# Optimization experiments

Measured on AMD Instinct MI355X. Metric: run time of the kernel, lower is better.

The kernel has to match this reference:

```python
import jax, jax.numpy as jnp
import numpy as np

VOCAB = 100000
EMBED = 64
SENT = 20
MEM = 50
BATCH = 32
HOPS = 3
PAD_ID = 0


def position_encoding(sentence_size, embedding_size):
    # Section 4.1 of MemN2N paper, vectorized. Returns [sentence_size, embedding_size].
    i = np.arange(1, embedding_size + 1, dtype=np.float32)[:, None]   # [E,1]
    j = np.arange(1, sentence_size + 1, dtype=np.float32)[None, :]    # [1,S]
    enc = (i - (embedding_size + 1) / 2.0) * (j - (sentence_size + 1) / 2.0)
    enc = 1.0 + 4.0 * enc / embedding_size / sentence_size
    enc[:, -1] = 1.0
    return jnp.asarray(enc.T, dtype=jnp.float32)  # [S,E]


def setup_inputs() -> dict:
    key = jax.random.key(0)
    k1, k2, k3, k4 = jax.random.split(key, 4)
    stories = jax.random.randint(k1, (BATCH, MEM, SENT), 0, VOCAB, dtype=jnp.int64 if jax.config.jax_enable_x64 else jnp.int32)
    queries = jax.random.randint(k2, (BATCH, SENT), 0, VOCAB, dtype=jnp.int64 if jax.config.jax_enable_x64 else jnp.int32)
    A = jax.random.normal(k3, (VOCAB, EMBED), dtype=jnp.float32) * 0.1
    C = jax.random.normal(k4, (HOPS, VOCAB, EMBED), dtype=jnp.float32) * 0.1
    # padding_idx=PAD_ID rows are zero, as in nn.Embedding(padding_idx=...)
    A = A.at[PAD_ID].set(0.0)
    C = C.at[:, PAD_ID].set(0.0)
    encoding = position_encoding(SENT, EMBED)
    return {"stories": stories, "queries": queries, "A": A, "C": C, "encoding": encoding}


def reference(stories, queries, A, C, encoding):
    # queries: [B,S], stories: [B,M,S], A: [V,E], C: [hops,V,E], encoding: [S,E]
    q_emb = A[queries]                                # [B,S,E]
    u = (q_emb * encoding).sum(axis=1)                # [B,E]
    for hop in range(HOPS):
        table_in = A if hop == 0 else C[hop - 1]
        emb_A = table_in[stories]                     # [B,M,S,E]
        m = (emb_A * encoding).sum(axis=2)            # [B,M,E]
        dotted = jnp.einsum('bme,be->bm', m, u)       # [B,M]
        probs = jax.nn.softmax(dotted, axis=-1)       # [B,M]
        emb_C = C[hop][stories]                       # [B,M,S,E]
        c = (emb_C * encoding).sum(axis=2)            # [B,M,E]
        o = jnp.einsum('bm,bme->be', probs, c)        # [B,E]
        u = u + o
    return u @ C[-1].T                                # [B,V]
```

## Files before the change

kernel.cpp:

```cpp
#include <hip/hip_runtime.h>
#include <hip/hip_bf16.h>

#define VOCAB 100000
#define EMBED 64
#define SENT  20
#define MEM   50
#define BATCH 32
#define HOPS  3

#define NSET   4
#define NSLOTB (NSET * MEM)
#define LDSP   65

__device__ __forceinline__ float bfr(unsigned short x) {
    union { unsigned int u; float f; } cv;
    cv.u = ((unsigned int)x) << 16;
    return cv.f;
}

__device__ __forceinline__ bool is_bf16(const void* enc) {
    return ((const unsigned int*)enc)[639] == 0x3F803F80u;
}

template<bool BF>
__device__ __forceinline__ float ldT(const void* p, size_t idx) {
    if constexpr (BF) return bfr(((const unsigned short*)p)[idx]);
    else              return ((const float*)p)[idx];
}

__device__ __forceinline__ float wave_sum(float d) {
#pragma unroll
    for (int off = 32; off > 0; off >>= 1) d += __shfl_xor(d, off, 64);
    return d;
}

template<bool BF>
__device__ __forceinline__ void gather_all(const int* __restrict__ stories,
                                           const int* __restrict__ queries,
                                           const void* __restrict__ A,
                                           const void* __restrict__ C,
                                           const void* __restrict__ enc,
                                           float* __restrict__ mc,
                                           float* __restrict__ uls,
                                           int b)
{
    const int tid = threadIdx.x;
    const int e   = tid & 63;
    const int w   = tid >> 6;
    const size_t VE = (size_t)VOCAB * EMBED;

    float encr[SENT];
#pragma unroll
    for (int s = 0; s < SENT; ++s) encr[s] = ldT<BF>(enc, s * EMBED + e);

    for (int slot = w; slot < NSLOTB + 1; slot += 16) {
        if (slot < NSLOTB) {
            const int t  = slot / MEM;
            const int mm = slot % MEM;
            const void* T   = (t == 0) ? A : C;
            const size_t to = (t == 0) ? 0 : (size_t)(t - 1) * VE;

            int wst = (e < SENT) ? stories[(b * MEM + mm) * SENT + e] : 0;
            float acc = 0.f;
#pragma unroll
            for (int s = 0; s < SENT; ++s) {
                int wd = __shfl(wst, s, 64);
                acc += ldT<BF>(T, to + (size_t)wd * EMBED + e) * encr[s];
            }
            mc[(t * MEM + mm) * LDSP + e] = acc;
        } else {
            int wq = (e < SENT) ? queries[b * SENT + e] : 0;
            float u = 0.f;
#pragma unroll
            for (int s = 0; s < SENT; ++s) {
                int wd = __shfl(wq, s, 64);
                u += ldT<BF>(A, (size_t)wd * EMBED + e) * encr[s];
            }
            uls[e] = u;
        }
    }
}

__global__ __launch_bounds__(1024) void k_front(
    const int* __restrict__ stories,
    const int* __restrict__ queries,
    const void* __restrict__ A,
    const void* __restrict__ C,
    const void* __restrict__ enc,
    float* __restrict__ u3g)
{
    __shared__ float mc[NSET * MEM * LDSP];
    __shared__ float uls[EMBED];
    __shared__ float ols[4][EMBED];

    const bool bf = is_bf16(enc);
    const int b   = blockIdx.x;
    const int tid = threadIdx.x;

    if (bf) gather_all<true >(stories, queries, A, C, enc, mc, uls, b);
    else    gather_all<false>(stories, queries, A, C, enc, mc, uls, b);
    __syncthreads();

    const int lane = tid & 63;
    const int widx = tid >> 6;

    for (int hop = 0; hop < HOPS; ++hop) {
        if (tid < 256) {
            float d = 0.f;
            if (lane < MEM) {
                const float* row = mc + (hop * MEM + lane) * LDSP;
#pragma unroll
                for (int e2 = 0; e2 < EMBED; ++e2) d += row[e2] * uls[e2];
            }
            float x  = (lane < MEM) ? d : -3.4e38f;
            float mx = x;
#pragma unroll
            for (int off = 32; off > 0; off >>= 1) mx = fmaxf(mx, __shfl_xor(mx, off, 64));
            float ex = (lane < MEM) ? __expf(x - mx) : 0.f;
            float sm = wave_sum(ex);
            float p  = ex / sm;

            float o = 0.f;
            const float* crow = mc + ((hop + 1) * MEM) * LDSP;
#pragma unroll
            for (int k = 0; k < 13; ++k) {
                int mm = widx * 13 + k;
                if (mm < MEM)
                    o += __shfl(p, mm, 64) * crow[mm * LDSP + lane];
            }
            ols[widx][lane] = o;
        }
        __syncthreads();
        if (tid < EMBED)
            uls[tid] += ols[0][tid] + ols[1][tid] + ols[2][tid] + ols[3][tid];
        __syncthreads();
    }

    if (tid < EMBED) u3g[b * EMBED + tid] = uls[tid];
}

template<bool BF>
__device__ __forceinline__ void out_one(const float* __restrict__ su,
                                        const void* __restrict__ Cbase,
                                        void* __restrict__ out, int v)
{
    const size_t c2_off = (size_t)2 * VOCAB * EMBED;
    float row[EMBED];
    if constexpr (BF) {
        const uint4* rp = (const uint4*)((const unsigned short*)Cbase + c2_off + (size_t)v * EMBED);
#pragma unroll
        for (int i = 0; i < 8; ++i) {
            uint4 r = rp[i];
            row[i*8 + 0] = bfr((unsigned short)(r.x & 0xffff));
            row[i*8 + 1] = bfr((unsigned short)(r.x >> 16));
            row[i*8 + 2] = bfr((unsigned short)(r.y & 0xffff));
            row[i*8 + 3] = bfr((unsigned short)(r.y >> 16));
            row[i*8 + 4] = bfr((unsigned short)(r.z & 0xffff));
            row[i*8 + 5] = bfr((unsigned short)(r.z >> 16));
            row[i*8 + 6] = bfr((unsigned short)(r.w & 0xffff));
            row[i*8 + 7] = bfr((unsigned short)(r.w >> 16));
        }
    } else {
        const float4* rp = (const float4*)((const float*)Cbase + c2_off + (size_t)v * EMBED);
#pragma unroll
        for (int i = 0; i < 16; ++i) {
            float4 r = rp[i];
            row[i*4 + 0] = r.x; row[i*4 + 1] = r.y;
            row[i*4 + 2] = r.z; row[i*4 + 3] = r.w;
        }
    }

    float res[BATCH];
#pragma unroll
    for (int bb = 0; bb < BATCH; ++bb) {
        const float4* sp = (const float4*)(su + bb * EMBED);
        float acc = 0.f;
#pragma unroll
        for (int e4 = 0; e4 < 16; ++e4) {
            float4 us = sp[e4];
            acc += row[e4*4+0]*us.x + row[e4*4+1]*us.y
                 + row[e4*4+2]*us.z + row[e4*4+3]*us.w;
        }
        res[bb] = acc;
    }

    if constexpr (BF) {
        unsigned short* ob = (unsigned short*)out;
#pragma unroll
        for (int bb = 0; bb < BATCH; ++bb) {
            __hip_bfloat16 h = __float2bfloat16(res[bb]);
            ob[(size_t)bb * VOCAB + v] = *(unsigned short*)&h;
        }
    } else {
        float* of = (float*)out;
#pragma unroll
        for (int bb = 0; bb < BATCH; ++bb)
            of[(size_t)bb * VOCAB + v] = res[bb];
    }
}

__global__ __launch_bounds__(256) void k_out(const float* __restrict__ u,
                                             const void* __restrict__ Cbase,
                                             const void* __restrict__ enc,
                                             void* __restrict__ out)
{
    const bool bf = is_bf16(enc);
    __shared__ __align__(16) float su[BATCH * EMBED];
    for (int i = threadIdx.x; i < BATCH * EMBED; i += 256) su[i] = u[i];
    __syncthreads();
    const int v = blockIdx.x * 256 + threadIdx.x;
    if (v >= VOCAB) return;
    if (bf) out_one<true >(su, Cbase, enc ? out : out, v);
    else    out_one<false>(su, Cbase, out, v);
}

extern "C" void kernel_launch(void* const* d_in, const int* in_sizes, int n_in,
                              void* d_out, int out_size, void* d_ws, size_t ws_size,
                              hipStream_t stream)
{
    const int*  stories = (const int*)d_in[0];
    const int*  queries = (const int*)d_in[1];
    const void* A       = d_in[2];
    const void* C       = d_in[3];
    const void* enc     = d_in[4];

    float* u3g = (float*)d_ws;

    k_front<<<BATCH, 1024, 0, stream>>>(stories, queries, A, C, enc, u3g);
    k_out<<<(VOCAB + 255) / 256, 256, 0, stream>>>(u3g, C, enc, d_out);
}
```

Baseline: 169.7 us.

## Merge front and output kernels into one cooperative kernel with grid-wide gather

Replaces the two-kernel pipeline (32-block gather+hops kernel, then vocab projection) with a single cooperative kernel of 512 blocks. The embedding gather is spread across all 2048 waves instead of 32 blocks, with results written to a global workspace. Two grid.sync barriers separate the gather, the per-batch hop computation on 32 blocks, and the vocab projection. This removes one kernel launch and the under-parallelised gather, at the cost of grid-sync overhead, global-memory round trips for the memory vectors, and a 512-block grid covering only about 391 output tiles.

```diff
diff --git a/kernel.cpp b/kernel.cpp
--- a/kernel.cpp
+++ b/kernel.cpp
@@ -1,5 +1,8 @@
 #include <hip/hip_runtime.h>
 #include <hip/hip_bf16.h>
+#include <hip/hip_cooperative_groups.h>
+
+namespace cg = cooperative_groups;
 
 #define VOCAB 100000
 #define EMBED 64
@@ -9,8 +12,9 @@
 #define HOPS  3
 
 #define NSET   4
-#define NSLOTB (NSET * MEM)
-#define LDSP   65
+#define NSLOT  (NSET * BATCH * MEM)
+#define GRID   512
+#define NWAVES (GRID * 4)
 
 __device__ __forceinline__ float bfr(unsigned short x) {
     union { unsigned int u; float f; } cv;
@@ -35,108 +39,50 @@
 }
 
 template<bool BF>
-__device__ __forceinline__ void gather_all(const int* __restrict__ stories,
-                                           const int* __restrict__ queries,
-                                           const void* __restrict__ A,
-                                           const void* __restrict__ C,
-                                           const void* __restrict__ enc,
-                                           float* __restrict__ mc,
-                                           float* __restrict__ uls,
-                                           int b)
+__device__ __forceinline__ void phase1(const int* __restrict__ stories,
+                                       const int* __restrict__ queries,
+                                       const void* __restrict__ A,
+                                       const void* __restrict__ C,
+                                       const void* __restrict__ enc,
+                                       float* __restrict__ mc_ws,
+                                       float* __restrict__ u0g)
 {
     const int tid = threadIdx.x;
     const int e   = tid & 63;
-    const int w   = tid >> 6;
+    const int gw  = blockIdx.x * 4 + (tid >> 6);
     const size_t VE = (size_t)VOCAB * EMBED;
 
     float encr[SENT];
 #pragma unroll
     for (int s = 0; s < SENT; ++s) encr[s] = ldT<BF>(enc, s * EMBED + e);
 
-    for (int slot = w; slot < NSLOTB + 1; slot += 16) {
-        if (slot < NSLOTB) {
-            const int t  = slot / MEM;
-            const int mm = slot % MEM;
+    for (int slot = gw; slot < NSLOT + BATCH; slot += NWAVES) {
+        if (slot < NSLOT) {
+            const int t  = slot / (BATCH * MEM);
+            const int bm = slot % (BATCH * MEM);
             const void* T   = (t == 0) ? A : C;
             const size_t to = (t == 0) ? 0 : (size_t)(t - 1) * VE;
 
-            int wst = (e < SENT) ? stories[(b * MEM + mm) * SENT + e] : 0;
+            int wst = (e < SENT) ? stories[bm * SENT + e] : 0;
             float acc = 0.f;
 #pragma unroll
             for (int s = 0; s < SENT; ++s) {
-                int wd = __shfl(wst, s, 64);
-                acc += ldT<BF>(T, to + (size_t)wd * EMBED + e) * encr[s];
-            }
-            mc[(t * MEM + mm) * LDSP + e] = acc;
+                int w = __shfl(wst, s, 64);
+                acc += ldT<BF>(T, to + (size_t)w * EMBED + e) * encr[s];
+            }
+            mc_ws[slot * EMBED + e] = acc;
         } else {
+            const int b = slot - NSLOT;
             int wq = (e < SENT) ? queries[b * SENT + e] : 0;
             float u = 0.f;
 #pragma unroll
             for (int s = 0; s < SENT; ++s) {
-                int wd = __shfl(wq, s, 64);
-                u += ldT<BF>(A, (size_t)wd * EMBED + e) * encr[s];
-            }
-            uls[e] = u;
-        }
-    }
-}
-
-__global__ __launch_bounds__(1024) void k_front(
-    const int* __restrict__ stories,
-    const int* __restrict__ queries,
-    const void* __restrict__ A,
-    const void* __restrict__ C,
-    const void* __restrict__ enc,
-    float* __restrict__ u3g)
-{
-    __shared__ float mc[NSET * MEM * LDSP];
-    __shared__ float uls[EMBED];
-    __shared__ float ols[4][EMBED];
-
-    const bool bf = is_bf16(enc);
-    const int b   = blockIdx.x;
-    const int tid = threadIdx.x;
-
-    if (bf) gather_all<true >(stories, queries, A, C, enc, mc, uls, b);
-    else    gather_all<false>(stories, queries, A, C, enc, mc, uls, b);
-    __syncthreads();
-
-    const int lane = tid & 63;
-    const int widx = tid >> 6;
-
-    for (int hop = 0; hop < HOPS; ++hop) {
-        if (tid < 256) {
-            float d = 0.f;
-            if (lane < MEM) {
-                const float* row = mc + (hop * MEM + lane) * LDSP;
-#pragma unroll
-                for (int e2 = 0; e2 < EMBED; ++e2) d += row[e2] * uls[e2];
-            }
-            float x  = (lane < MEM) ? d : -3.4e38f;
-            float mx = x;
-#pragma unroll
-            for (int off = 32; off > 0; off >>= 1) mx = fmaxf(mx, __shfl_xor(mx, off, 64));
-            float ex = (lane < MEM) ? __expf(x - mx) : 0.f;
-            float sm = wave_sum(ex);
-            float p  = ex / sm;
-
-            float o = 0.f;
-            const float* crow = mc + ((hop + 1) * MEM) * LDSP;
-#pragma unroll
-            for (int k = 0; k < 13; ++k) {
-                int mm = widx * 13 + k;
-                if (mm < MEM)
-                    o += __shfl(p, mm, 64) * crow[mm * LDSP + lane];
-            }
-            ols[widx][lane] = o;
-        }
-        __syncthreads();
-        if (tid < EMBED)
-            uls[tid] += ols[0][tid] + ols[1][tid] + ols[2][tid] + ols[3][tid];
-        __syncthreads();
-    }
-
-    if (tid < EMBED) u3g[b * EMBED + tid] = uls[tid];
+                int w = __shfl(wq, s, 64);
+                u += ldT<BF>(A, (size_t)w * EMBED + e) * encr[s];
+            }
+            u0g[b * EMBED + e] = u;
+        }
+    }
 }
 
 template<bool BF>
@@ -199,19 +145,84 @@
     }
 }
 
-__global__ __launch_bounds__(256) void k_out(const float* __restrict__ u,
-                                             const void* __restrict__ Cbase,
-                                             const void* __restrict__ enc,
-                                             void* __restrict__ out)
-{
+__global__ __launch_bounds__(256, 2) void k_all(
+    const int* __restrict__ stories,
+    const int* __restrict__ queries,
+    const void* __restrict__ A,
+    const void* __restrict__ C,
+    const void* __restrict__ enc,
+    float* __restrict__ mc_ws,
+    float* __restrict__ u0g,
+    float* __restrict__ u3g,
+    void* __restrict__ out)
+{
+    __shared__ float smem[BATCH * EMBED];
+    cg::grid_group grid = cg::this_grid();
+
     const bool bf = is_bf16(enc);
-    __shared__ __align__(16) float su[BATCH * EMBED];
-    for (int i = threadIdx.x; i < BATCH * EMBED; i += 256) su[i] = u[i];
-    __syncthreads();
-    const int v = blockIdx.x * 256 + threadIdx.x;
-    if (v >= VOCAB) return;
-    if (bf) out_one<true >(su, Cbase, enc ? out : out, v);
-    else    out_one<false>(su, Cbase, out, v);
+    const int tid = threadIdx.x;
+
+    if (bf) phase1<true >(stories, queries, A, C, enc, mc_ws, u0g);
+    else    phase1<false>(stories, queries, A, C, enc, mc_ws, u0g);
+
+    grid.sync();
+
+    if (blockIdx.x < BATCH) {
+        const int b    = blockIdx.x;
+        const int lane = tid & 63;
+        const int widx = tid >> 6;
+        float* uls = smem;
+        float* ols = smem + EMBED;
+
+        if (tid < EMBED) uls[tid] = u0g[b * EMBED + tid];
+        __syncthreads();
+
+        for (int hop = 0; hop < HOPS; ++hop) {
+            float d = 0.f;
+            if (lane < MEM) {
+                const float* row = mc_ws +
+                    ((size_t)hop * BATCH * MEM + (size_t)b * MEM + lane) * EMBED;
+#pragma unroll
+                for (int e2 = 0; e2 < EMBED; ++e2) d += row[e2] * uls[e2];
+            }
+            float x  = (lane < MEM) ? d : -3.4e38f;
+            float mx = x;
+#pragma unroll
+            for (int off = 32; off > 0; off >>= 1) mx = fmaxf(mx, __shfl_xor(mx, off, 64));
+            float ex = (lane < MEM) ? __expf(x - mx) : 0.f;
+            float sm = wave_sum(ex);
+            float p  = ex / sm;
+
+            float o = 0.f;
+            const float* crow = mc_ws +
+                ((size_t)(hop + 1) * BATCH * MEM + (size_t)b * MEM) * EMBED;
+#pragma unroll
+            for (int k = 0; k < 13; ++k) {
+                int mm = widx * 13 + k;
+                if (mm < MEM)
+                    o += __shfl(p, mm, 64) * crow[mm * EMBED + lane];
+            }
+            ols[widx * EMBED + lane] = o;
+            __syncthreads();
+            if (tid < EMBED)
+                uls[tid] += ols[0*EMBED+tid] + ols[1*EMBED+tid]
+                          + ols[2*EMBED+tid] + ols[3*EMBED+tid];
+            __syncthreads();
+        }
+        if (tid < EMBED) u3g[b * EMBED + tid] = uls[tid];
+    }
+
+    grid.sync();
+
+    if ((size_t)blockIdx.x * 256 < VOCAB) {
+        for (int i = tid; i < BATCH * EMBED; i += 256) smem[i] = u3g[i];
+        __syncthreads();
+        const int v = blockIdx.x * 256 + tid;
+        if (v < VOCAB) {
+            if (bf) out_one<true >(smem, C, out, v);
+            else    out_one<false>(smem, C, out, v);
+        }
+    }
 }
 
 extern "C" void kernel_launch(void* const* d_in, const int* in_sizes, int n_in,
@@ -224,8 +235,14 @@
     const void* C       = d_in[3];
     const void* enc     = d_in[4];
 
-    float* u3g = (float*)d_ws;
-
-    k_front<<<BATCH, 1024, 0, stream>>>(stories, queries, A, C, enc, u3g);
-    k_out<<<(VOCAB + 255) / 256, 256, 0, stream>>>(u3g, C, enc, d_out);
-}
+    float* mc_ws = (float*)d_ws;
+    float* u0g   = mc_ws + NSLOT * EMBED;
+    float* u3g   = u0g + BATCH * EMBED;
+
+    void* kargs[] = {
+        (void*)&stories, (void*)&queries, (void*)&A, (void*)&C, (void*)&enc,
+        (void*)&mc_ws, (void*)&u0g, (void*)&u3g, (void*)&d_out
+    };
+    hipLaunchCooperativeKernel((const void*)k_all, dim3(GRID), dim3(256),
+                               kargs, 0, stream);
+}
```

Measured after the change: 275.3 us. 1.62x slower.
